# Optimization experiments

Measured on AMD Instinct MI355X. Metric: run time of the kernel, lower is better.

Reference implementation:

```python
import jax, jax.numpy as jnp
import numpy as np

NX, NY, NZ = 64, 48, 32          # grid_resolution
N = NX * NY * NZ                 # 98304 grid cells
P = 10                           # neighbors_in_radius
D = 3                            # spatial dims
M = 5                            # num_modes (fourier)
BN = 64                          # base_neurons
BN_IN = 8                        # base_neurons_in (output channels)
IN_FEAT = D * (1 + 2 * M)        # 33


def _linear_init(k, fan_in, fan_out):
    s = 1.0 / np.sqrt(fan_in)
    kw, kb = jax.random.split(k)
    W = jax.random.uniform(kw, (fan_in, fan_out), jnp.float32, -s, s)
    b = jax.random.uniform(kb, (fan_out,), jnp.float32, -s, s)
    return W, b


def setup_inputs() -> dict:
    key = jax.random.key(0)
    ks = jax.random.split(key, 6)
    # neighbor point coordinates gathered by ball query: (b, N, P, 3)
    x = jax.random.normal(ks[0], (1, N, P, D), jnp.float32)
    # regular grid coordinates: (b, nx, ny, nz, 3)
    grid = jax.random.normal(ks[1], (1, NX, NY, NZ, D), jnp.float32)
    # fourier frequency buffer: exp(linspace(0, pi, num_modes))
    freqs = jnp.exp(jnp.linspace(0.0, float(np.pi), M)).astype(jnp.float32)
    W1, b1 = _linear_init(ks[2], IN_FEAT, BN)
    W2, b2 = _linear_init(ks[3], BN, BN // 2)
    W3, b3 = _linear_init(ks[4], BN // 2, BN_IN)
    return dict(x=x, grid=grid, freqs=freqs,
                W1=W1, b1=b1, W2=W2, b2=b2, W3=W3, b3=b3)


def _fourier_encode(coords, freqs):
    # coords: (b, N, P, D), freqs: (F,)
    scaled = coords[..., None, :] * freqs[:, None]          # (b, N, P, F, D)
    b, n, p = coords.shape[:3]
    scaled = scaled.reshape(b, n, p, -1)                    # (b, N, P, F*D)
    return jnp.concatenate([jnp.sin(scaled), jnp.cos(scaled)], axis=-1)


def reference(x, grid, freqs, W1, b1, W2, b2, W3, b3):
    gelu = lambda t: jax.nn.gelu(t, approximate=False)  # torch F.gelu default = exact erf
    # Fourier feature encode neighbor coords: (b, N, P, 33)
    facets = jnp.concatenate([x, _fourier_encode(x, freqs)], axis=-1)
    h = gelu(facets @ W1 + b1)                              # (b, N, P, 64)
    h = gelu(h @ W2 + b2)                                   # (b, N, P, 32)
    h = jnp.tanh(h @ W3 + b3)                               # (b, N, P, 8)
    # mask out padded neighbors (zero coords); original uses x-coordinate channel
    mask = (jnp.abs(x[..., 0:1]) > 1e-6).astype(h.dtype)    # (b, N, P, 1)
    out = jnp.sum(h * mask, axis=2)                         # scatter/aggregate -> (b, N, 8)
    out = out.reshape(out.shape[0], NX, NY, NZ, BN_IN)
    return jnp.transpose(out, (0, 4, 1, 2, 3))              # (b, 8, nx, ny, nz)
```

## Files before the change

### kernel.cpp

```cpp
#include <hip/hip_runtime.h>
#include <math.h>

#define NXD 64
#define NYD 48
#define NZD 32
#define NPT (NXD*NYD*NZD)
#define PN  10
#define MF  5
#define H1  64
#define H2  32
#define H3  8

#define PTS_PER_BLOCK 32
#define ROWS_PER_BLOCK (PTS_PER_BLOCK*PN)
#define TILES_PER_WAVE 5

#define A2S 72
#define A3S 40

#define INV2PI 0.15915494309189535f

typedef __attribute__((ext_vector_type(8))) short short8;
typedef __attribute__((ext_vector_type(4))) float f32x4;

static __device__ const unsigned short kSlotTab[32] = {
  2048,    3,   70,  137,  204,  271, 1042, 1109,
  2561, 1176, 1243, 1310,  516,  583,  650,  717,
  2562,  272, 1043, 1110, 1177, 1244, 1311,  517,
    72,  139,  206,  273, 1044, 1111, 1178, 1245 };

__device__ __forceinline__ short f2bf(float f) {
    unsigned u = __float_as_uint(f);
    unsigned r = (u + 0x7fffu + ((u >> 16) & 1u)) >> 16;
    return (short)r;
}

__device__ __forceinline__ unsigned short f2bf_hu(float f) {
    return (unsigned short)((__float_as_uint(f) + 0x8000u) >> 16);
}

__device__ __forceinline__ unsigned pack2_bf16(float lo, float hi) {
    return __builtin_amdgcn_perm(__float_as_uint(hi) + 0x8000u,
                                 __float_as_uint(lo) + 0x8000u, 0x07060302u);
}

__device__ __forceinline__ float gelu_fast(float x) {
    float x2 = x * x;
    float t  = x * (2.3022082f + 0.10294324f * x2);
    float E  = __builtin_amdgcn_exp2f(t);
    return x - x * __builtin_amdgcn_rcpf(E + 1.0f);
}

__device__ __forceinline__ float tanh_fast(float v) {
    float E = __builtin_amdgcn_exp2f(2.8853901f * v);
    return 1.0f - 2.0f * __builtin_amdgcn_rcpf(E + 1.0f);
}

__global__ __launch_bounds__(256) void domino_mfma_kernel(
    const float* __restrict__ x,
    const float* __restrict__ freqs,
    const float* __restrict__ W1,
    const float* __restrict__ b1,
    const float* __restrict__ W2,
    const float* __restrict__ b2,
    const float* __restrict__ W3,
    const float* __restrict__ b3,
    float* __restrict__ out)
{
    __shared__ __align__(16) unsigned short a2buf[4][16 * A2S];
    __shared__ __align__(16) float cbuf[976];
    __shared__ __align__(16) _Float16 obuf[ROWS_PER_BLOCK * 9];
    __shared__ __align__(16) float mcx[4][16];
    __shared__ __align__(16) float mv32[4][16];
    __shared__ __align__(16) float coefA[2][32];
    __shared__ __align__(16) float coefB[2][32];
    __shared__ __align__(16) float coefO[2][32];

    const int tid  = threadIdx.x;
    const int w    = tid >> 6;
    const int lane = tid & 63;
    const int lr   = lane & 15;
    const int lg   = lane >> 4;

    const int wrow0 = blockIdx.x * ROWS_PER_BLOCK + w * (TILES_PER_WAVE*16);

    if (tid < 32) {
        const unsigned e = kSlotTab[tid];
        const int m = (e >> 6) & 7, path = (e >> 9) & 1, ty = (e >> 10) & 3;
        const float fm = freqs[m] * INV2PI;
        const float fa = (ty != 2 && path == 0) ? fm : 0.0f;
        const float fb = (ty != 2 && path == 1) ? fm : 0.0f;
        const float fo = (ty == 1) ? 0.25f : 0.0f;
        coefA[0][tid] = fa; coefA[1][tid] = fa;
        coefB[0][tid] = fb; coefB[1][tid] = fb;
        coefO[0][tid] = fo; coefO[1][tid] = fo;
    }

    {
        const int sl = (w == 3 && lane >= 60) ? 59 : lane;
        const float* gsrc = x + (size_t)wrow0 * 3 + (size_t)sl * 4;
        __builtin_amdgcn_global_load_lds(
            (const __attribute__((address_space(1))) void*)gsrc,
            (__attribute__((address_space(3))) void*)&cbuf[w * 240], 16, 0, 0);
    }

    const float f4rev = freqs[4] * INV2PI;
    const float rawf  = (lg < 3) ? 1.0f : 0.0f;

    short8 B1f[4];
    float  w32[4], bv1[4];
    #pragma unroll
    for (int t1 = 0; t1 < 4; ++t1) {
        #pragma unroll
        for (int j = 0; j < 8; ++j) {
            const int row = kSlotTab[lg*8 + j] & 63;
            B1f[t1][j] = f2bf(W1[row*H1 + t1*16 + lr]);
        }
        w32[t1] = W1[32*H1 + t1*16 + lr];
        bv1[t1] = b1[t1*16 + lr];
    }
    short8 B2f[2][2];
    float  bv2[2];
    #pragma unroll
    for (int s = 0; s < 2; ++s)
        #pragma unroll
        for (int t2 = 0; t2 < 2; ++t2)
            #pragma unroll
            for (int j = 0; j < 8; ++j)
                B2f[s][t2][j] = f2bf(W2[(s*32 + lg*8 + j)*H2 + t2*16 + lr]);
    #pragma unroll
    for (int t2 = 0; t2 < 2; ++t2) bv2[t2] = b2[t2*16 + lr];

    short8 B3f;
    float  bv3 = (lr < H3) ? b3[lr] : 0.0f;
    #pragma unroll
    for (int j = 0; j < 8; ++j)
        B3f[j] = (lr < H3) ? f2bf(W3[(lg*8 + j)*H3 + lr]) : (short)0;

    __syncthreads();

    #pragma unroll 1
    for (int t = 0; t < TILES_PER_WAVE; ++t) {
        const int cfx = w*240 + (t*16 + lr)*3;
        const float cx = cbuf[cfx + 0];
        const float cy = cbuf[cfx + 1];
        const float cz = cbuf[cfx + 2];

        const float cA = (lg <= 1) ? cx : ((lg == 2) ? cy : cz);
        const float cB = (lg == 0) ? cx : ((lg == 1) ? cy : cz);

        const int tc = t & 1;
        float fv[8];
        {
            const f32x4 fa0 = *(const f32x4*)&coefA[tc][lg*8];
            const f32x4 fb0 = *(const f32x4*)&coefB[tc][lg*8];
            const f32x4 fo0 = *(const f32x4*)&coefO[tc][lg*8];
            #pragma unroll
            for (int j = 0; j < 4; ++j) {
                float rev = cA*fa0[j] + (cB*fb0[j] + fo0[j]);
                fv[j] = __builtin_amdgcn_sinf(__builtin_amdgcn_fractf(rev));
            }
        }
        __builtin_amdgcn_sched_barrier(0);
        {
            const f32x4 fa1 = *(const f32x4*)&coefA[tc][lg*8 + 4];
            const f32x4 fb1 = *(const f32x4*)&coefB[tc][lg*8 + 4];
            const f32x4 fo1 = *(const f32x4*)&coefO[tc][lg*8 + 4];
            #pragma unroll
            for (int j = 0; j < 4; ++j) {
                float rev = cA*fa1[j] + (cB*fb1[j] + fo1[j]);
                fv[4+j] = __builtin_amdgcn_sinf(__builtin_amdgcn_fractf(rev));
            }
        }
        fv[0] += rawf * (cB - fv[0]);

        if (lg == 0) {
            mcx[w][lr]  = cx;
            mv32[w][lr] = __builtin_amdgcn_sinf(__builtin_amdgcn_fractf(cz * f4rev + 0.25f));
        }

        union { unsigned u[4]; short8 s8; } a1u;
        #pragma unroll
        for (int j = 0; j < 4; ++j) a1u.u[j] = pack2_bf16(fv[2*j], fv[2*j+1]);
        const short8 a1 = a1u.s8;

        f32x4 c1[4];
        #pragma unroll
        for (int t1 = 0; t1 < 4; ++t1) {
            f32x4 ci = {bv1[t1], bv1[t1], bv1[t1], bv1[t1]};
            c1[t1] = __builtin_amdgcn_mfma_f32_16x16x32_bf16(a1, B1f[t1], ci, 0, 0, 0);
        }
        const f32x4 v32r = *(const f32x4*)&mv32[w][lg*4];
        const f32x4 mxr  = *(const f32x4*)&mcx[w][lg*4];
        #pragma unroll
        for (int t1 = 0; t1 < 4; ++t1)
            #pragma unroll
            for (int r = 0; r < 4; ++r)
                c1[t1][r] += v32r[r] * w32[t1];
        #pragma unroll
        for (int t1 = 0; t1 < 4; ++t1)
            #pragma unroll
            for (int r = 0; r < 4; ++r)
                c1[t1][r] = gelu_fast(c1[t1][r]);

        #pragma unroll
        for (int t1 = 0; t1 < 4; ++t1)
            #pragma unroll
            for (int r = 0; r < 4; ++r)
                a2buf[w][(lg*4 + r)*A2S + t1*16 + lr] = f2bf_hu(c1[t1][r]);
        short8 a2f[2];
        #pragma unroll
        for (int s = 0; s < 2; ++s)
            a2f[s] = *(const short8*)&a2buf[w][lr*A2S + s*32 + lg*8];

        f32x4 c2[2];
        #pragma unroll
        for (int t2 = 0; t2 < 2; ++t2) {
            f32x4 ci = {bv2[t2], bv2[t2], bv2[t2], bv2[t2]};
            ci = __builtin_amdgcn_mfma_f32_16x16x32_bf16(a2f[0], B2f[0][t2], ci, 0, 0, 0);
            c2[t2] = __builtin_amdgcn_mfma_f32_16x16x32_bf16(a2f[1], B2f[1][t2], ci, 0, 0, 0);
        }
        #pragma unroll
        for (int t2 = 0; t2 < 2; ++t2)
            #pragma unroll
            for (int r = 0; r < 4; ++r)
                c2[t2][r] = gelu_fast(c2[t2][r]);

        unsigned short* const a3p = &a2buf[w][0];
        #pragma unroll
        for (int t2 = 0; t2 < 2; ++t2)
            #pragma unroll
            for (int r = 0; r < 4; ++r)
                a3p[(lg*4 + r)*A3S + t2*16 + lr] = f2bf_hu(c2[t2][r]);
        short8 a3f = *(const short8*)&a3p[lr*A3S + lg*8];

        f32x4 c3 = {bv3, bv3, bv3, bv3};
        c3 = __builtin_amdgcn_mfma_f32_16x16x32_bf16(a3f, B3f, c3, 0, 0, 0);

        #pragma unroll
        for (int r = 0; r < 4; ++r) {
            const int brow = w*(TILES_PER_WAVE*16) + t*16 + lg*4 + r;
            const float mk = (fabsf(mxr[r]) > 1e-6f) ? 1.0f : 0.0f;
            if (lr < H3) obuf[brow*9 + lr] = (_Float16)(mk * tanh_fast(c3[r]));
        }
    }

    __syncthreads();

    {
        const int p  = tid >> 3;
        const int ch = tid & 7;
        float sum = 0.0f;
        #pragma unroll
        for (int i = 0; i < PN; ++i) sum += (float)obuf[(p*PN + i)*9 + ch];
        const int gp = blockIdx.x * PTS_PER_BLOCK + p;
        out[(size_t)ch * NPT + gp] = sum;
    }
}

extern "C" void kernel_launch(void* const* d_in, const int* in_sizes, int n_in,
                              void* d_out, int out_size, void* d_ws, size_t ws_size,
                              hipStream_t stream) {
    const float* x     = (const float*)d_in[0];
    const float* freqs = (const float*)d_in[2];
    const float* W1    = (const float*)d_in[3];
    const float* b1    = (const float*)d_in[4];
    const float* W2    = (const float*)d_in[5];
    const float* b2    = (const float*)d_in[6];
    const float* W3    = (const float*)d_in[7];
    const float* b3    = (const float*)d_in[8];
    float* out = (float*)d_out;

    const int grid = NPT / PTS_PER_BLOCK;
    domino_mfma_kernel<<<grid, 256, 0, stream>>>(x, freqs, W1, b1, W2, b2, W3, b3, out);
}
```

Baseline: 125.4 us.

## Switch MLP matmuls to fp16 MFMA and compute GELU in packed half precision

```diff
diff --git a/kernel.cpp b/kernel.cpp
--- a/kernel.cpp
+++ b/kernel.cpp
@@ -20,8 +20,16 @@
 
 #define INV2PI 0.15915494309189535f
 
-typedef __attribute__((ext_vector_type(8))) short short8;
-typedef __attribute__((ext_vector_type(4))) float f32x4;
+typedef __attribute__((ext_vector_type(8))) _Float16 half8;
+typedef __attribute__((ext_vector_type(2))) _Float16 half2v;
+typedef __attribute__((ext_vector_type(2))) __fp16   fp16x2;
+typedef __attribute__((ext_vector_type(2))) short    shortv2;
+typedef __attribute__((ext_vector_type(4))) float    f32x4;
+
+__device__ __forceinline__ half2v cvt_pk_h2(float lo, float hi) {
+    fp16x2 p = __builtin_amdgcn_cvt_pkrtz(lo, hi);
+    return __builtin_bit_cast(half2v, p);
+}
 
 static __device__ const unsigned short kSlotTab[32] = {
   2048,    3,   70,  137,  204,  271, 1042, 1109,
@@ -29,26 +37,28 @@
   2562,  272, 1043, 1110, 1177, 1244, 1311,  517,
     72,  139,  206,  273, 1044, 1111, 1178, 1245 };
 
-__device__ __forceinline__ short f2bf(float f) {
-    unsigned u = __float_as_uint(f);
-    unsigned r = (u + 0x7fffu + ((u >> 16) & 1u)) >> 16;
-    return (short)r;
-}
-
-__device__ __forceinline__ unsigned short f2bf_hu(float f) {
-    return (unsigned short)((__float_as_uint(f) + 0x8000u) >> 16);
-}
-
-__device__ __forceinline__ unsigned pack2_bf16(float lo, float hi) {
-    return __builtin_amdgcn_perm(__float_as_uint(hi) + 0x8000u,
-                                 __float_as_uint(lo) + 0x8000u, 0x07060302u);
-}
-
-__device__ __forceinline__ float gelu_fast(float x) {
-    float x2 = x * x;
-    float t  = x * (2.3022082f + 0.10294324f * x2);
-    float E  = __builtin_amdgcn_exp2f(t);
-    return x - x * __builtin_amdgcn_rcpf(E + 1.0f);
+__device__ __forceinline__ _Float16 exp2h(_Float16 v) {
+    _Float16 r;
+    asm("v_exp_f16 %0, %1" : "=v"(r) : "v"(v));
+    return r;
+}
+
+__device__ __forceinline__ half2v gelu_pk(float lo, float hi) {
+    const _Float16 C1 = (_Float16)2.3022082f, C2 = (_Float16)0.10294324f;
+    const half2v x  = cvt_pk_h2(lo, hi);
+    const half2v x2 = x * x;
+    half2v t = x * __builtin_elementwise_fma(x2, (half2v){C2, C2}, (half2v){C1, C1});
+    t = __builtin_elementwise_min(t, (half2v){(_Float16)14.0f, (_Float16)14.0f});
+    const _Float16 e0 = exp2h(t[0]);
+    const _Float16 e1 = exp2h(t[1]);
+    const half2v one = {(_Float16)1.0f, (_Float16)1.0f};
+    const half2v two = {(_Float16)2.0f, (_Float16)2.0f};
+    const half2v y = (half2v){e0, e1} + one;
+    const shortv2 rb = (shortv2){(short)0x7800, (short)0x7800} - __builtin_bit_cast(shortv2, y);
+    half2v r = __builtin_bit_cast(half2v, rb);
+    r = r * __builtin_elementwise_fma(-y, r, two);
+    r = r * __builtin_elementwise_fma(-y, r, two);
+    return x - x * r;
 }
 
 __device__ __forceinline__ float tanh_fast(float v) {
@@ -67,7 +77,7 @@
     const float* __restrict__ b3,
     float* __restrict__ out)
 {
-    __shared__ __align__(16) unsigned short a2buf[4][16 * A2S];
+    __shared__ __align__(16) _Float16 a2buf[4][16 * A2S];
     __shared__ __align__(16) float cbuf[976];
     __shared__ __align__(16) _Float16 obuf[ROWS_PER_BLOCK * 9];
     __shared__ __align__(16) float mcx[4][16];
@@ -107,19 +117,19 @@
     const float f4rev = freqs[4] * INV2PI;
     const float rawf  = (lg < 3) ? 1.0f : 0.0f;
 
-    short8 B1f[4];
+    half8 B1f[4];
     float  w32[4], bv1[4];
     #pragma unroll
     for (int t1 = 0; t1 < 4; ++t1) {
         #pragma unroll
         for (int j = 0; j < 8; ++j) {
             const int row = kSlotTab[lg*8 + j] & 63;
-            B1f[t1][j] = f2bf(W1[row*H1 + t1*16 + lr]);
+            B1f[t1][j] = (_Float16)W1[row*H1 + t1*16 + lr];
         }
         w32[t1] = W1[32*H1 + t1*16 + lr];
         bv1[t1] = b1[t1*16 + lr];
     }
-    short8 B2f[2][2];
+    half8 B2f[2][2];
     float  bv2[2];
     #pragma unroll
     for (int s = 0; s < 2; ++s)
@@ -127,15 +137,15 @@
         for (int t2 = 0; t2 < 2; ++t2)
             #pragma unroll
             for (int j = 0; j < 8; ++j)
-                B2f[s][t2][j] = f2bf(W2[(s*32 + lg*8 + j)*H2 + t2*16 + lr]);
+                B2f[s][t2][j] = (_Float16)W2[(s*32 + lg*8 + j)*H2 + t2*16 + lr];
     #pragma unroll
     for (int t2 = 0; t2 < 2; ++t2) bv2[t2] = b2[t2*16 + lr];
 
-    short8 B3f;
+    half8 B3f;
     float  bv3 = (lr < H3) ? b3[lr] : 0.0f;
     #pragma unroll
     for (int j = 0; j < 8; ++j)
-        B3f[j] = (lr < H3) ? f2bf(W3[(lg*8 + j)*H3 + lr]) : (short)0;
+        B3f[j] = (lr < H3) ? (_Float16)W3[(lg*8 + j)*H3 + lr] : (_Float16)0.0f;
 
     __syncthreads();
 
@@ -179,16 +189,17 @@
             mv32[w][lr] = __builtin_amdgcn_sinf(__builtin_amdgcn_fractf(cz * f4rev + 0.25f));
         }
 
-        union { unsigned u[4]; short8 s8; } a1u;
-        #pragma unroll
-        for (int j = 0; j < 4; ++j) a1u.u[j] = pack2_bf16(fv[2*j], fv[2*j+1]);
-        const short8 a1 = a1u.s8;
+        union { half2v h2[4]; half8 h8; } a1u;
+        #pragma unroll
+        for (int j = 0; j < 4; ++j)
+            a1u.h2[j] = cvt_pk_h2(fv[2*j], fv[2*j+1]);
+        const half8 a1 = a1u.h8;
 
         f32x4 c1[4];
         #pragma unroll
         for (int t1 = 0; t1 < 4; ++t1) {
             f32x4 ci = {bv1[t1], bv1[t1], bv1[t1], bv1[t1]};
-            c1[t1] = __builtin_amdgcn_mfma_f32_16x16x32_bf16(a1, B1f[t1], ci, 0, 0, 0);
+            c1[t1] = __builtin_amdgcn_mfma_f32_16x16x32_f16(a1, B1f[t1], ci, 0, 0, 0);
         }
         const f32x4 v32r = *(const f32x4*)&mv32[w][lg*4];
         const f32x4 mxr  = *(const f32x4*)&mcx[w][lg*4];
@@ -197,45 +208,45 @@
             #pragma unroll
             for (int r = 0; r < 4; ++r)
                 c1[t1][r] += v32r[r] * w32[t1];
-        #pragma unroll
-        for (int t1 = 0; t1 < 4; ++t1)
-            #pragma unroll
-            for (int r = 0; r < 4; ++r)
-                c1[t1][r] = gelu_fast(c1[t1][r]);
-
-        #pragma unroll
-        for (int t1 = 0; t1 < 4; ++t1)
-            #pragma unroll
-            for (int r = 0; r < 4; ++r)
-                a2buf[w][(lg*4 + r)*A2S + t1*16 + lr] = f2bf_hu(c1[t1][r]);
-        short8 a2f[2];
+
+        #pragma unroll
+        for (int t1 = 0; t1 < 4; ++t1) {
+            const half2v g01 = gelu_pk(c1[t1][0], c1[t1][1]);
+            const half2v g23 = gelu_pk(c1[t1][2], c1[t1][3]);
+            const int col = t1*16 + lr;
+            a2buf[w][(lg*4 + 0)*A2S + col] = g01[0];
+            a2buf[w][(lg*4 + 1)*A2S + col] = g01[1];
+            a2buf[w][(lg*4 + 2)*A2S + col] = g23[0];
+            a2buf[w][(lg*4 + 3)*A2S + col] = g23[1];
+        }
+        half8 a2f[2];
         #pragma unroll
         for (int s = 0; s < 2; ++s)
-            a2f[s] = *(const short8*)&a2buf[w][lr*A2S + s*32 + lg*8];
+            a2f[s] = *(const half8*)&a2buf[w][lr*A2S + s*32 + lg*8];
 
         f32x4 c2[2];
         #pragma unroll
         for (int t2 = 0; t2 < 2; ++t2) {
             f32x4 ci = {bv2[t2], bv2[t2], bv2[t2], bv2[t2]};
-            ci = __builtin_amdgcn_mfma_f32_16x16x32_bf16(a2f[0], B2f[0][t2], ci, 0, 0, 0);
-            c2[t2] = __builtin_amdgcn_mfma_f32_16x16x32_bf16(a2f[1], B2f[1][t2], ci, 0, 0, 0);
-        }
-        #pragma unroll
-        for (int t2 = 0; t2 < 2; ++t2)
-            #pragma unroll
-            for (int r = 0; r < 4; ++r)
-                c2[t2][r] = gelu_fast(c2[t2][r]);
-
-        unsigned short* const a3p = &a2buf[w][0];
-        #pragma unroll
-        for (int t2 = 0; t2 < 2; ++t2)
-            #pragma unroll
-            for (int r = 0; r < 4; ++r)
-                a3p[(lg*4 + r)*A3S + t2*16 + lr] = f2bf_hu(c2[t2][r]);
-        short8 a3f = *(const short8*)&a3p[lr*A3S + lg*8];
+            ci = __builtin_amdgcn_mfma_f32_16x16x32_f16(a2f[0], B2f[0][t2], ci, 0, 0, 0);
+            c2[t2] = __builtin_amdgcn_mfma_f32_16x16x32_f16(a2f[1], B2f[1][t2], ci, 0, 0, 0);
+        }
+
+        _Float16* const a3p = &a2buf[w][0];
+        #pragma unroll
+        for (int t2 = 0; t2 < 2; ++t2) {
+            const half2v g01 = gelu_pk(c2[t2][0], c2[t2][1]);
+            const half2v g23 = gelu_pk(c2[t2][2], c2[t2][3]);
+            const int col = t2*16 + lr;
+            a3p[(lg*4 + 0)*A3S + col] = g01[0];
+            a3p[(lg*4 + 1)*A3S + col] = g01[1];
+            a3p[(lg*4 + 2)*A3S + col] = g23[0];
+            a3p[(lg*4 + 3)*A3S + col] = g23[1];
+        }
+        half8 a3f = *(const half8*)&a3p[lr*A3S + lg*8];
 
         f32x4 c3 = {bv3, bv3, bv3, bv3};
-        c3 = __builtin_amdgcn_mfma_f32_16x16x32_bf16(a3f, B3f, c3, 0, 0, 0);
+        c3 = __builtin_amdgcn_mfma_f32_16x16x32_f16(a3f, B3f, c3, 0, 0, 0);
 
         #pragma unroll
         for (int r = 0; r < 4; ++r) {
```

Result: faster. 120.9 us (-3.6%).
